# Optimization experiments

Measured on AMD Instinct MI355X. Metric: run time of the kernel, lower is better.

Reference implementation:

```python
import jax, jax.numpy as jnp
import numpy as np

EMBED_DIM = 1024
NHEAD = 16
HEAD_DIM = EMBED_DIM // NHEAD
BASE = 10000.0


def rope_tables(seq_len, dim):
    # dim = head_dim; freqs over dim/2
    inv_freq = 1.0 / (BASE ** (jnp.arange(0, dim, 2, dtype=jnp.float32) / dim))
    t = jnp.arange(seq_len, dtype=jnp.float32)
    freqs = jnp.einsum('i,j->ij', t, inv_freq)          # [S, dim/2]
    return jnp.cos(freqs), jnp.sin(freqs)


def apply_rope(x, cos, sin):
    # x: [B,H,S,D]; cos/sin: [S, D/2] broadcast over B,H
    x1, x2 = jnp.split(x, 2, axis=-1)
    return jnp.concatenate((x1 * cos - x2 * sin, x1 * sin + x2 * cos), axis=-1)


def setup_inputs() -> dict:
    key = jax.random.key(0)
    ks = jax.random.split(key, 7)
    B, S, E = 2, 2048, EMBED_DIM
    scale = 1.0 / np.sqrt(E)
    return {
        'query': jax.random.normal(ks[0], (B, S, E), dtype=jnp.float32),
        'key':   jax.random.normal(ks[1], (B, S, E), dtype=jnp.float32),
        'value': jax.random.normal(ks[2], (B, S, E), dtype=jnp.float32),
        'Wq': jax.random.normal(ks[3], (E, E), dtype=jnp.float32) * scale,
        'Wk': jax.random.normal(ks[4], (E, E), dtype=jnp.float32) * scale,
        'Wv': jax.random.normal(ks[5], (E, E), dtype=jnp.float32) * scale,
        'Wo': jax.random.normal(ks[6], (E, E), dtype=jnp.float32) * scale,
    }


def reference(query, key, value, Wq, Wk, Wv, Wo):
    B, Sq, E = query.shape
    Skv = key.shape[1]
    H, D = NHEAD, HEAD_DIM
    # projections (nn.Linear: x @ W.T), split heads -> [B,H,S,D]
    q = (query @ Wq.T).reshape(B, Sq, H, D).transpose(0, 2, 1, 3)
    k = (key   @ Wk.T).reshape(B, Skv, H, D).transpose(0, 2, 1, 3)
    v = (value @ Wv.T).reshape(B, Skv, H, D).transpose(0, 2, 1, 3)
    cos, sin = rope_tables(Sq, D)
    q = apply_rope(q, cos, sin)
    k = apply_rope(k, cos, sin)
    scores = jnp.einsum('bhqd,bhkd->bhqk', q, k) / jnp.sqrt(jnp.asarray(D, q.dtype))
    probs = jax.nn.softmax(scores, axis=-1)
    out = jnp.einsum('bhqk,bhkd->bhqd', probs, v)
    out = out.transpose(0, 2, 1, 3).reshape(B, Sq, E)
    return out @ Wo.T
```

## Files before the change

### kernel.cpp

```cpp
#include <hip/hip_runtime.h>

typedef __bf16 bf16_t;
typedef __attribute__((ext_vector_type(8))) __bf16 bf16x8;
typedef __attribute__((ext_vector_type(4))) __bf16 bf16x4;
typedef __attribute__((ext_vector_type(4))) float f32x4;
typedef __attribute__((ext_vector_type(16))) float f32x16;
typedef __attribute__((ext_vector_type(4))) int i32x4;

#define GAS __attribute__((address_space(1)))
#define LAS __attribute__((address_space(3)))

__device__ __forceinline__ void gload_lds16(const bf16_t* g, bf16_t* l) {
  __builtin_amdgcn_global_load_lds((const GAS char*)(const char*)g,
                                   (LAS char*)(char*)l, 16, 0, 0);
}

__global__ __launch_bounds__(256) void f2bf_all(const float* __restrict__ q,
                                                const float* __restrict__ k,
                                                const float* __restrict__ v,
                                                const float* __restrict__ wq,
                                                const float* __restrict__ wk,
                                                const float* __restrict__ wv,
                                                const float* __restrict__ wo,
                                                bf16_t* __restrict__ ws,
                                                float* __restrict__ ct,
                                                float* __restrict__ st) {
  if (blockIdx.x >= 16384) {
    const int gid = (blockIdx.x - 16384) * 256 + threadIdx.x;
    const int s = gid >> 5, j = gid & 31;
    const float inv = exp2f(-(float)j * (13.287712379549449f / 32.0f));
    const float ang = (float)s * inv;
    ct[gid] = cosf(ang);
    st[gid] = sinf(ang);
    return;
  }
  const size_t T = 4194304, W = 1048576;
  const size_t gid = (size_t)(blockIdx.x * 256 + threadIdx.x) * 4;
  const float* src; bf16_t* dst; size_t off;
  if      (gid < T)         { src = q;  off = gid;             dst = ws; }
  else if (gid < 2*T)       { src = k;  off = gid - T;         dst = ws + T; }
  else if (gid < 3*T)       { src = v;  off = gid - 2*T;       dst = ws + 2*T; }
  else if (gid < 3*T + W)   { src = wq; off = gid - 3*T;       dst = ws + 3*T; }
  else if (gid < 3*T + 2*W) { src = wk; off = gid - 3*T - W;   dst = ws + 3*T + W; }
  else if (gid < 3*T + 3*W) { src = wv; off = gid - 3*T - 2*W; dst = ws + 3*T + 2*W; }
  else                      { src = wo; off = gid - 3*T - 3*W; dst = ws + 3*T + 3*W; }
  const float4 vv = *(const float4*)(src + off);
  bf16x4 o;
  o[0] = (bf16_t)vv.x; o[1] = (bf16_t)vv.y; o[2] = (bf16_t)vv.z; o[3] = (bf16_t)vv.w;
  *(bf16x4*)(dst + off) = o;
}

template <int EPI>
__device__ __forceinline__ void gemm_bt_body(const bf16_t* __restrict__ A,
                                             const bf16_t* __restrict__ Bm,
                                             void* __restrict__ Cout,
                                             const float* __restrict__ ctab,
                                             const float* __restrict__ stab,
                                             const float scale,
                                             const int m0, const int n0) {
  constexpr int K = 1024, N = 1024;
  __shared__ __align__(16) bf16_t sm[17408];
  bf16_t* As = sm;
  bf16_t* Bs = sm + 8192;
  const int tid = threadIdx.x;
  const int lane = tid & 63;
  const int w = tid >> 6;
  const int wr = w >> 1, wc = w & 1;
  const int g = lane >> 4, c = lane & 15;

  f32x4 acc[4][4] = {};

  for (int k0 = 0; k0 < K; k0 += 64) {
#pragma unroll
    for (int i = 0; i < 4; ++i) {
      const int chunk0 = (i * 4 + w) * 64;
      const int idx = chunk0 + lane;
      const int row = idx >> 3;
      const int sw = (idx & 7) ^ (row & 7);
      gload_lds16(A  + (size_t)(m0 + row) * K + (k0 + sw * 8), As + chunk0 * 8);
      gload_lds16(Bm + (size_t)(n0 + row) * K + (k0 + sw * 8), Bs + chunk0 * 8);
    }
    __syncthreads();
    bf16x8 af[4][2], bfr[4][2];
#pragma unroll
    for (int t = 0; t < 4; ++t) {
#pragma unroll
      for (int kc = 0; kc < 2; ++kc) {
        const int ra = wr * 64 + t * 16 + c;
        af[t][kc] = *(const bf16x8*)(As + ra * 64 + (((kc * 4 + g) ^ (ra & 7)) * 8));
        const int rb = wc * 64 + t * 16 + c;
        bfr[t][kc] = *(const bf16x8*)(Bs + rb * 64 + (((kc * 4 + g) ^ (rb & 7)) * 8));
      }
    }
#pragma unroll
    for (int mi = 0; mi < 4; ++mi)
#pragma unroll
      for (int ni = 0; ni < 4; ++ni)
#pragma unroll
        for (int kc = 0; kc < 2; ++kc)
          acc[mi][ni] = __builtin_amdgcn_mfma_f32_16x16x32_bf16(
              af[mi][kc], bfr[ni][kc], acc[mi][ni], 0, 0, 0);
    __syncthreads();
  }
  if (EPI == 2) {
#pragma unroll
    for (int mi = 0; mi < 4; ++mi)
#pragma unroll
      for (int ni = 0; ni < 4; ++ni)
#pragma unroll
        for (int r = 0; r < 4; ++r) {
          const int lr = wr * 64 + mi * 16 + g * 4 + r;
          const int lc = wc * 64 + ni * 16 + c;
          sm[lc * 136 + lr] = (bf16_t)acc[mi][ni][r];
        }
    __syncthreads();
    bf16_t* Vt = (bf16_t*)Cout;
    const int bb = m0 >> 11, sbase = m0 & 2047;
#pragma unroll
    for (int it = 0; it < 8; ++it) {
      const int idx = it * 256 + tid;
      const int lc = idx >> 4, kk = idx & 15;
      const bf16x8 vv = *(const bf16x8*)(sm + lc * 136 + kk * 8);
      *(bf16x8*)(Vt + ((size_t)(bb * 1024 + n0 + lc)) * 2048 + sbase + kk * 8) = vv;
    }
    return;
  }
  if (EPI == 0 && ctab != nullptr) {
    bf16_t* Cb = (bf16_t*)Cout;
#pragma unroll
    for (int mi = 0; mi < 4; ++mi)
#pragma unroll
      for (int r = 0; r < 4; ++r) {
        const int grow = m0 + wr * 64 + mi * 16 + g * 4 + r;
        const int s = grow & 2047;
        const float* crow = ctab + s * 32;
        const float* srow = stab + s * 32;
#pragma unroll
        for (int ni = 0; ni < 2; ++ni) {
          const int j = ni * 16 + c;
          const float cc = crow[j], ss = srow[j];
          const float x1 = acc[mi][ni][r];
          const float x2 = acc[mi][ni + 2][r];
          const int gcol = n0 + wc * 64 + j;
          Cb[(size_t)grow * N + gcol]      = (bf16_t)((x1 * cc - x2 * ss) * scale);
          Cb[(size_t)grow * N + gcol + 32] = (bf16_t)((x1 * ss + x2 * cc) * scale);
        }
      }
    return;
  }
#pragma unroll
  for (int mi = 0; mi < 4; ++mi)
#pragma unroll
    for (int ni = 0; ni < 4; ++ni)
#pragma unroll
      for (int r = 0; r < 4; ++r) {
        const int grow = m0 + wr * 64 + mi * 16 + g * 4 + r;
        const int gcol = n0 + wc * 64 + ni * 16 + c;
        const float v = acc[mi][ni][r];
        if (EPI == 0) ((bf16_t*)Cout)[(size_t)grow * N + gcol] = (bf16_t)v;
        else          ((float*)Cout)[(size_t)grow * N + gcol] = v;
      }
}

__global__ __launch_bounds__(256) void qkv_gemm(
    const bf16_t* __restrict__ qb, const bf16_t* __restrict__ kb, const bf16_t* __restrict__ vb,
    const bf16_t* __restrict__ wqb, const bf16_t* __restrict__ wkb, const bf16_t* __restrict__ wvb,
    bf16_t* __restrict__ Qp, bf16_t* __restrict__ Kp, bf16_t* __restrict__ Vtp,
    const float* __restrict__ ctab, const float* __restrict__ stab) {
  const int bid = blockIdx.x;
  const int wg = (bid & 7) * 96 + (bid >> 3);
  const int z = wg >> 8;
  const int rem = wg & 255;
  const int m0 = (rem >> 3) * 128;
  const int n0 = (rem & 7) * 128;
  if (z == 0) {
    gemm_bt_body<0>(qb, wqb, Qp, ctab, stab, 0.18033688011112042f, m0, n0);
  } else if (z == 1) {
    gemm_bt_body<0>(kb, wkb, Kp, ctab, stab, 1.0f, m0, n0);
  } else {
    gemm_bt_body<2>(vb, wvb, Vtp, nullptr, nullptr, 1.0f, m0, n0);
  }
}

__global__ __launch_bounds__(256) void out_gemm(const bf16_t* __restrict__ A,
                                                const bf16_t* __restrict__ B,
                                                float* __restrict__ C) {
  const int bid = blockIdx.x;
  const int wg = (bid & 7) * 32 + (bid >> 3);
  const int m0 = (wg >> 3) * 128;
  const int n0 = (wg & 7) * 128;
  gemm_bt_body<1>(A, B, C, nullptr, nullptr, 1.0f, m0, n0);
}

__global__ __launch_bounds__(512, 4) void flash_attn(const bf16_t* __restrict__ Q,
                                                     const bf16_t* __restrict__ Kr,
                                                     const bf16_t* __restrict__ Vt,
                                                     bf16_t* __restrict__ O) {
  __shared__ __align__(16) bf16_t Ksm[2][2][64 * 64];
  __shared__ __align__(16) bf16_t Vsm[2][2][64 * 64];
  const int tid = threadIdx.x, lane = tid & 63, w = tid >> 6;
  const int wl = w & 3, g = w >> 2;
  const int li = lane & 31, hi = lane >> 5;
  const int bid = blockIdx.x;
  const int xcd = bid & 7, slot = bid >> 3;
  const int bh = xcd * 4 + (slot >> 4);
  const int qb = slot & 15;
  const int b = bh >> 4, h = bh & 15;
  const int q0 = qb * 128 + wl * 32;

  bf16x8 qf[4];
  {
    const size_t qaddr = ((size_t)b * 2048 + q0 + li) * 1024 + h * 64 + hi * 8;
#pragma unroll
    for (int ks = 0; ks < 4; ++ks) qf[ks] = *(const bf16x8*)(Q + qaddr + ks * 16);
  }

  bf16x8 ones;
#pragma unroll
  for (int j = 0; j < 8; ++j) ones[j] = (bf16_t)1.0f;

  const f32x16 zero16 = {};
  f32x16 o0 = zero16, o1 = zero16, osum = zero16;

  const size_t kbase  = (size_t)b * 2048 * 1024 + h * 64;
  const size_t vtbase = (size_t)((b * 16 + h) * 64) * 2048;
  const int kv_off = g * 1024;

#define STAGE(buf, kv0)                                                          \
  {                                                                              \
    _Pragma("unroll")                                                            \
    for (int i = 0; i < 2; ++i) {                                                \
      const int chunk0 = (i * 4 + wl) * 64;                                      \
      const int idx = chunk0 + lane;                                             \
      const int row = idx >> 3;                                                  \
      const int sw = ((idx & 7) ^ (row & 7)) * 8;                                \
      gload_lds16(Kr + kbase + (size_t)((kv0) + row) * 1024 + sw,                \
                  &Ksm[g][buf][chunk0 * 8]);                                     \
      gload_lds16(Vt + vtbase + (size_t)row * 2048 + (kv0) + sw,                 \
                  &Vsm[g][buf][chunk0 * 8]);                                     \
    }                                                                            \
  }

#define CVTPK(dst, lo_, hi_) \
  asm("v_cvt_pk_bf16_f32 %0, %1, %2" : "=v"(dst) : "v"(lo_), "v"(hi_))
#define PLSWAP(x_, y_) \
  asm volatile("v_permlane32_swap_b32 %0, %1" : "+v"(x_), "+v"(y_))

  STAGE(0, kv_off)
  asm volatile("s_waitcnt vmcnt(0)" ::: "memory");
  __builtin_amdgcn_s_barrier();
  int cur = 0;
  for (int t = 0; t < 16; ++t) {
    if (t < 15) STAGE(cur ^ 1, kv_off + (t + 1) * 64)

    f32x16 p0 = zero16, p1 = zero16;
    __builtin_amdgcn_s_setprio(1);
#pragma unroll
    for (int ks = 0; ks < 4; ++ks) {
      const int r0 = li;
      const bf16x8 kf0 = *(const bf16x8*)(&Ksm[g][cur][r0 * 64 + (((ks * 2 + hi) ^ (r0 & 7)) * 8)]);
      p0 = __builtin_amdgcn_mfma_f32_32x32x16_bf16(kf0, qf[ks], p0, 0, 0, 0);
      const int r1 = 32 + li;
      const bf16x8 kf1 = *(const bf16x8*)(&Ksm[g][cur][r1 * 64 + (((ks * 2 + hi) ^ (r1 & 7)) * 8)]);
      p1 = __builtin_amdgcn_mfma_f32_32x32x16_bf16(kf1, qf[ks], p1, 0, 0, 0);
    }
    __builtin_amdgcn_s_setprio(0);

#pragma unroll
    for (int j = 0; j < 16; ++j) { p0[j] = exp2f(p0[j]); p1[j] = exp2f(p1[j]); }

    bf16x8 pa[4];
#pragma unroll
    for (int ks = 0; ks < 4; ++ks) {
      int A_, B_, C_, D_;
      if (ks == 0) { CVTPK(A_, p0[0], p0[1]); CVTPK(B_, p0[2], p0[3]);
                     CVTPK(C_, p0[4], p0[5]); CVTPK(D_, p0[6], p0[7]); }
      else if (ks == 1) { CVTPK(A_, p0[8],  p0[9]);  CVTPK(B_, p0[10], p0[11]);
                          CVTPK(C_, p0[12], p0[13]); CVTPK(D_, p0[14], p0[15]); }
      else if (ks == 2) { CVTPK(A_, p1[0], p1[1]); CVTPK(B_, p1[2], p1[3]);
                          CVTPK(C_, p1[4], p1[5]); CVTPK(D_, p1[6], p1[7]); }
      else { CVTPK(A_, p1[8],  p1[9]);  CVTPK(B_, p1[10], p1[11]);
             CVTPK(C_, p1[12], p1[13]); CVTPK(D_, p1[14], p1[15]); }
      PLSWAP(A_, C_);
      PLSWAP(B_, D_);
      i32x4 iv; iv[0] = A_; iv[1] = B_; iv[2] = C_; iv[3] = D_;
      pa[ks] = __builtin_bit_cast(bf16x8, iv);
    }

    __builtin_amdgcn_s_setprio(1);
#pragma unroll
    for (int ks = 0; ks < 4; ++ks) {
      const int r0 = li;
      const bf16x8 vf0 = *(const bf16x8*)(&Vsm[g][cur][r0 * 64 + (((ks * 2 + hi) ^ (r0 & 7)) * 8)]);
      o0 = __builtin_amdgcn_mfma_f32_32x32x16_bf16(pa[ks], vf0, o0, 0, 0, 0);
      const int r1 = 32 + li;
      const bf16x8 vf1 = *(const bf16x8*)(&Vsm[g][cur][r1 * 64 + (((ks * 2 + hi) ^ (r1 & 7)) * 8)]);
      o1 = __builtin_amdgcn_mfma_f32_32x32x16_bf16(pa[ks], vf1, o1, 0, 0, 0);
      osum = __builtin_amdgcn_mfma_f32_32x32x16_bf16(pa[ks], ones, osum, 0, 0, 0);
    }
    __builtin_amdgcn_s_setprio(0);

    if (t < 15) {
      asm volatile("s_waitcnt vmcnt(0)" ::: "memory");
      __builtin_amdgcn_s_barrier();
    }
    cur ^= 1;
  }
#undef STAGE
#undef CVTPK
#undef PLSWAP

  float* Osm = (float*)&Ksm[0][0][0];
  float* lsm = (float*)&Vsm[0][0][0];

  if (g == 1) {
    float* Ow = Osm + wl * 2048;
#pragma unroll
    for (int reg = 0; reg < 16; ++reg) {
      const int ql = (reg & 3) + 8 * (reg >> 2) + 4 * hi;
      Ow[ql * 64 + li]      = o0[reg];
      Ow[ql * 64 + 32 + li] = o1[reg];
      if (li == 0) lsm[wl * 32 + ql] = osum[reg];
    }
  }
  __syncthreads();
  if (g == 0) {
    const float* Ow = Osm + wl * 2048;
#pragma unroll
    for (int reg = 0; reg < 16; ++reg) {
      const int ql = (reg & 3) + 8 * (reg >> 2) + 4 * hi;
      const float rl = 1.0f / (osum[reg] + lsm[wl * 32 + ql]);
      const size_t base = ((size_t)b * 2048 + q0 + ql) * 1024 + h * 64 + li;
      O[base]      = (bf16_t)((o0[reg] + Ow[ql * 64 + li])      * rl);
      O[base + 32] = (bf16_t)((o1[reg] + Ow[ql * 64 + 32 + li]) * rl);
    }
  }
}

extern "C" void kernel_launch(void* const* d_in, const int* in_sizes, int n_in,
                              void* d_out, int out_size, void* d_ws, size_t ws_size,
                              hipStream_t stream) {
  (void)in_sizes; (void)n_in; (void)out_size; (void)ws_size;
  const float* q_in = (const float*)d_in[0];
  const float* k_in = (const float*)d_in[1];
  const float* v_in = (const float*)d_in[2];
  const float* wq = (const float*)d_in[3];
  const float* wk = (const float*)d_in[4];
  const float* wv = (const float*)d_in[5];
  const float* wo = (const float*)d_in[6];
  float* out = (float*)d_out;

  bf16_t* ws = (bf16_t*)d_ws;
  const size_t T = 4096ull * 1024ull;
  const size_t W = 1024ull * 1024ull;
  bf16_t* qb  = ws;
  bf16_t* kb  = qb + T;
  bf16_t* vb  = kb + T;
  bf16_t* wqb = vb + T;
  bf16_t* wkb = wqb + W;
  bf16_t* wvb = wkb + W;
  bf16_t* wob = wvb + W;
  bf16_t* Qp  = wob + W;
  bf16_t* Kp  = Qp + T;
  bf16_t* Vtp = Kp + T;
  bf16_t* AO  = Vtp + T;
  float* ctab = (float*)(AO + T);
  float* stab = ctab + 65536;

  f2bf_all<<<16640, 256, 0, stream>>>(q_in, k_in, v_in, wq, wk, wv, wo, ws, ctab, stab);
  qkv_gemm<<<768, 256, 0, stream>>>(qb, kb, vb, wqb, wkb, wvb, Qp, Kp, Vtp, ctab, stab);
  flash_attn<<<512, 512, 0, stream>>>(Qp, Kp, Vtp, AO);
  out_gemm<<<256, 256, 0, stream>>>(AO, wob, out);
}
```

Baseline: 138.6 us.

## Fuse fp32-to-bf16 activation conversion into QKV GEMM A-operand loads

The conversion kernel now handles only the weights and the RoPE tables. The QKV GEMM reads the fp32 activations directly into registers, converts them to bf16 and writes them into swizzled LDS, prefetching the next k-tile into registers after the barrier. This removes a full write and read of the 3x4M bf16 activation copies through global memory. In exchange it adds register pressure (8 float4 per thread) and synchronous LDS stores in place of async global-to-LDS loads, and each fp32 activation tile is converted 8 times, once per N-tile block.

After: 129.8 us. 6.3% less time.

```diff
diff --git a/kernel.cpp b/kernel.cpp
--- a/kernel.cpp
+++ b/kernel.cpp
@@ -15,18 +15,15 @@
                                    (LAS char*)(char*)l, 16, 0, 0);
 }
 
-__global__ __launch_bounds__(256) void f2bf_all(const float* __restrict__ q,
-                                                const float* __restrict__ k,
-                                                const float* __restrict__ v,
-                                                const float* __restrict__ wq,
-                                                const float* __restrict__ wk,
-                                                const float* __restrict__ wv,
-                                                const float* __restrict__ wo,
-                                                bf16_t* __restrict__ ws,
-                                                float* __restrict__ ct,
-                                                float* __restrict__ st) {
-  if (blockIdx.x >= 16384) {
-    const int gid = (blockIdx.x - 16384) * 256 + threadIdx.x;
+__global__ __launch_bounds__(256) void f2bf_w(const float* __restrict__ wq,
+                                              const float* __restrict__ wk,
+                                              const float* __restrict__ wv,
+                                              const float* __restrict__ wo,
+                                              bf16_t* __restrict__ wsb,
+                                              float* __restrict__ ct,
+                                              float* __restrict__ st) {
+  if (blockIdx.x >= 4096) {
+    const int gid = (blockIdx.x - 4096) * 256 + threadIdx.x;
     const int s = gid >> 5, j = gid & 31;
     const float inv = exp2f(-(float)j * (13.287712379549449f / 32.0f));
     const float ang = (float)s * inv;
@@ -34,24 +31,21 @@
     st[gid] = sinf(ang);
     return;
   }
-  const size_t T = 4194304, W = 1048576;
+  const size_t W = 1048576;
   const size_t gid = (size_t)(blockIdx.x * 256 + threadIdx.x) * 4;
-  const float* src; bf16_t* dst; size_t off;
-  if      (gid < T)         { src = q;  off = gid;             dst = ws; }
-  else if (gid < 2*T)       { src = k;  off = gid - T;         dst = ws + T; }
-  else if (gid < 3*T)       { src = v;  off = gid - 2*T;       dst = ws + 2*T; }
-  else if (gid < 3*T + W)   { src = wq; off = gid - 3*T;       dst = ws + 3*T; }
-  else if (gid < 3*T + 2*W) { src = wk; off = gid - 3*T - W;   dst = ws + 3*T + W; }
-  else if (gid < 3*T + 3*W) { src = wv; off = gid - 3*T - 2*W; dst = ws + 3*T + 2*W; }
-  else                      { src = wo; off = gid - 3*T - 3*W; dst = ws + 3*T + 3*W; }
+  const float* src; size_t off;
+  if      (gid < W)     { src = wq; off = gid; }
+  else if (gid < 2 * W) { src = wk; off = gid - W; }
+  else if (gid < 3 * W) { src = wv; off = gid - 2 * W; }
+  else                  { src = wo; off = gid - 3 * W; }
   const float4 vv = *(const float4*)(src + off);
   bf16x4 o;
   o[0] = (bf16_t)vv.x; o[1] = (bf16_t)vv.y; o[2] = (bf16_t)vv.z; o[3] = (bf16_t)vv.w;
-  *(bf16x4*)(dst + off) = o;
-}
-
-template <int EPI>
-__device__ __forceinline__ void gemm_bt_body(const bf16_t* __restrict__ A,
+  *(bf16x4*)(wsb + gid) = o;
+}
+
+template <int EPI, int AF32>
+__device__ __forceinline__ void gemm_bt_body(const void* __restrict__ Ap,
                                              const bf16_t* __restrict__ Bm,
                                              void* __restrict__ Cout,
                                              const float* __restrict__ ctab,
@@ -67,20 +61,61 @@
   const int w = tid >> 6;
   const int wr = w >> 1, wc = w & 1;
   const int g = lane >> 4, c = lane & 15;
+  const bf16_t* Ab = (const bf16_t*)Ap;
+  const float* Af = (const float*)Ap;
 
   f32x4 acc[4][4] = {};
 
+  float4 areg[8];
+  if (AF32) {
+#pragma unroll
+    for (int i = 0; i < 8; ++i) {
+      const int idx4 = i * 256 + tid;
+      const int row = idx4 >> 4, c4 = idx4 & 15;
+      areg[i] = *(const float4*)(Af + (size_t)(m0 + row) * K + c4 * 4);
+    }
+  }
+
   for (int k0 = 0; k0 < K; k0 += 64) {
-#pragma unroll
-    for (int i = 0; i < 4; ++i) {
-      const int chunk0 = (i * 4 + w) * 64;
-      const int idx = chunk0 + lane;
-      const int row = idx >> 3;
-      const int sw = (idx & 7) ^ (row & 7);
-      gload_lds16(A  + (size_t)(m0 + row) * K + (k0 + sw * 8), As + chunk0 * 8);
-      gload_lds16(Bm + (size_t)(n0 + row) * K + (k0 + sw * 8), Bs + chunk0 * 8);
+    if (AF32) {
+#pragma unroll
+      for (int i = 0; i < 8; ++i) {
+        const int idx4 = i * 256 + tid;
+        const int row = idx4 >> 4, c4 = idx4 & 15;
+        const int sw8 = (c4 >> 1) ^ (row & 7);
+        bf16x4 o;
+        o[0] = (bf16_t)areg[i].x; o[1] = (bf16_t)areg[i].y;
+        o[2] = (bf16_t)areg[i].z; o[3] = (bf16_t)areg[i].w;
+        *(bf16x4*)(As + row * 64 + sw8 * 8 + (c4 & 1) * 4) = o;
+      }
+#pragma unroll
+      for (int i = 0; i < 4; ++i) {
+        const int chunk0 = (i * 4 + w) * 64;
+        const int idx = chunk0 + lane;
+        const int row = idx >> 3;
+        const int sw = (idx & 7) ^ (row & 7);
+        gload_lds16(Bm + (size_t)(n0 + row) * K + (k0 + sw * 8), Bs + chunk0 * 8);
+      }
+    } else {
+#pragma unroll
+      for (int i = 0; i < 4; ++i) {
+        const int chunk0 = (i * 4 + w) * 64;
+        const int idx = chunk0 + lane;
+        const int row = idx >> 3;
+        const int sw = (idx & 7) ^ (row & 7);
+        gload_lds16(Ab + (size_t)(m0 + row) * K + (k0 + sw * 8), As + chunk0 * 8);
+        gload_lds16(Bm + (size_t)(n0 + row) * K + (k0 + sw * 8), Bs + chunk0 * 8);
+      }
     }
     __syncthreads();
+    if (AF32 && k0 + 64 < K) {
+#pragma unroll
+      for (int i = 0; i < 8; ++i) {
+        const int idx4 = i * 256 + tid;
+        const int row = idx4 >> 4, c4 = idx4 & 15;
+        areg[i] = *(const float4*)(Af + (size_t)(m0 + row) * K + (k0 + 64) + c4 * 4);
+      }
+    }
     bf16x8 af[4][2], bfr[4][2];
 #pragma unroll
     for (int t = 0; t < 4; ++t) {
@@ -163,7 +198,7 @@
 }
 
 __global__ __launch_bounds__(256) void qkv_gemm(
-    const bf16_t* __restrict__ qb, const bf16_t* __restrict__ kb, const bf16_t* __restrict__ vb,
+    const float* __restrict__ qf, const float* __restrict__ kf, const float* __restrict__ vf,
     const bf16_t* __restrict__ wqb, const bf16_t* __restrict__ wkb, const bf16_t* __restrict__ wvb,
     bf16_t* __restrict__ Qp, bf16_t* __restrict__ Kp, bf16_t* __restrict__ Vtp,
     const float* __restrict__ ctab, const float* __restrict__ stab) {
@@ -174,11 +209,11 @@
   const int m0 = (rem >> 3) * 128;
   const int n0 = (rem & 7) * 128;
   if (z == 0) {
-    gemm_bt_body<0>(qb, wqb, Qp, ctab, stab, 0.18033688011112042f, m0, n0);
+    gemm_bt_body<0, 1>(qf, wqb, Qp, ctab, stab, 0.18033688011112042f, m0, n0);
   } else if (z == 1) {
-    gemm_bt_body<0>(kb, wkb, Kp, ctab, stab, 1.0f, m0, n0);
+    gemm_bt_body<0, 1>(kf, wkb, Kp, ctab, stab, 1.0f, m0, n0);
   } else {
-    gemm_bt_body<2>(vb, wvb, Vtp, nullptr, nullptr, 1.0f, m0, n0);
+    gemm_bt_body<2, 1>(vf, wvb, Vtp, nullptr, nullptr, 1.0f, m0, n0);
   }
 }
 
@@ -189,7 +224,7 @@
   const int wg = (bid & 7) * 32 + (bid >> 3);
   const int m0 = (wg >> 3) * 128;
   const int n0 = (wg & 7) * 128;
-  gemm_bt_body<1>(A, B, C, nullptr, nullptr, 1.0f, m0, n0);
+  gemm_bt_body<1, 0>(A, B, C, nullptr, nullptr, 1.0f, m0, n0);
 }
 
 __global__ __launch_bounds__(512, 4) void flash_attn(const bf16_t* __restrict__ Q,
@@ -353,10 +388,7 @@
   bf16_t* ws = (bf16_t*)d_ws;
   const size_t T = 4096ull * 1024ull;
   const size_t W = 1024ull * 1024ull;
-  bf16_t* qb  = ws;
-  bf16_t* kb  = qb + T;
-  bf16_t* vb  = kb + T;
-  bf16_t* wqb = vb + T;
+  bf16_t* wqb = ws;
   bf16_t* wkb = wqb + W;
   bf16_t* wvb = wkb + W;
   bf16_t* wob = wvb + W;
@@ -367,8 +399,9 @@
   float* ctab = (float*)(AO + T);
   float* stab = ctab + 65536;
 
-  f2bf_all<<<16640, 256, 0, stream>>>(q_in, k_in, v_in, wq, wk, wv, wo, ws, ctab, stab);
-  qkv_gemm<<<768, 256, 0, stream>>>(qb, kb, vb, wqb, wkb, wvb, Qp, Kp, Vtp, ctab, stab);
+  f2bf_w<<<4352, 256, 0, stream>>>(wq, wk, wv, wo, wqb, ctab, stab);
+  qkv_gemm<<<768, 256, 0, stream>>>(q_in, k_in, v_in, wqb, wkb, wvb, Qp, Kp, Vtp,
+                                    ctab, stab);
   flash_attn<<<512, 512, 0, stream>>>(Qp, Kp, Vtp, AO);
   out_gemm<<<256, 256, 0, stream>>>(AO, wob, out);
 }
```
